# Kernel tuning notes

Hardware: AMD Instinct MI355X
Metric: run time of the kernel (lower is better)

Reference implementation:

```python
import jax, jax.numpy as jnp
import numpy as np

N_NODES = 50000
N_EDGES = 800000
D_FEAT = 64


def setup_inputs() -> dict:
    key = jax.random.key(0)
    k1, k2, k3, k4 = jax.random.split(key, 4)
    rows = jnp.sort(jax.random.randint(k1, (N_EDGES,), 0, N_NODES, dtype=jnp.int64))
    cols = jax.random.randint(k2, (N_EDGES,), 0, N_NODES, dtype=jnp.int64)
    vals = jax.random.uniform(k3, (N_EDGES,), dtype=jnp.float32)
    embeds = jax.random.normal(k4, (N_NODES, D_FEAT), dtype=jnp.float32)
    return {"rows": rows, "cols": cols, "vals": vals, "embeds": embeds}


def reference(rows, cols, vals, embeds):
    # torch.spmm(adj, embeds) with adj in COO form:
    # out[r] = sum_{e: rows[e]==r} vals[e] * embeds[cols[e]]
    gathered = vals[:, None] * embeds[cols]            # [E, D]
    out = jax.ops.segment_sum(gathered, rows, num_segments=N_NODES)  # [N, D]
    return out
```

## Files before the change

### kernel.cpp

```cpp
#include <hip/hip_runtime.h>
#include <hip/hip_fp16.h>


#define D_FEAT 64
#define BLOCK 256

typedef float f32x4 __attribute__((ext_vector_type(4)));

__global__ __launch_bounds__(BLOCK) void setup_fused(
    const int* __restrict__ rows, int* __restrict__ row_ptr,
    const float* __restrict__ embeds, __half* __restrict__ embeds_h,
    int n_nodes, int n_edges, int n4, int nb_rp)
{
    if ((int)blockIdx.x < nb_rp) {
        const int e = blockIdx.x * BLOCK + threadIdx.x;
        if (e >= n_edges) return;
        const int r  = rows[e];
        const int rp = (e == 0) ? -1 : rows[e - 1];
        for (int v = rp + 1; v <= r; ++v) row_ptr[v] = e;
        if (e == n_edges - 1)
            for (int v = r + 1; v <= n_nodes; ++v) row_ptr[v] = n_edges;
    } else {
        const int i = ((int)blockIdx.x - nb_rp) * BLOCK + (int)threadIdx.x;
        if (i >= n4) return;
        const float4 x = ((const float4*)embeds)[i];
        __half2 a = __floats2half2_rn(x.x, x.y);
        __half2 b = __floats2half2_rn(x.z, x.w);
        ((__half2*)embeds_h)[2 * i]     = a;
        ((__half2*)embeds_h)[2 * i + 1] = b;
    }
}

__global__ __launch_bounds__(BLOCK) void spmm_row_f16(
    const int* __restrict__ row_ptr,
    const int* __restrict__ cols,
    const float* __restrict__ vals,
    const __half* __restrict__ embeds_h,
    float* __restrict__ out,
    int n_nodes)
{
    const int wave = (int)((blockIdx.x * (unsigned)BLOCK + threadIdx.x) >> 6);
    if (wave >= n_nodes) return;
    const int lane = (int)(threadIdx.x & 63u);
    const int slot = lane >> 3;
    const int f8   = lane & 7;

    const int s = row_ptr[wave];
    const int t = row_ptr[wave + 1];

    float acc[8] = {0.f, 0.f, 0.f, 0.f, 0.f, 0.f, 0.f, 0.f};

    const char* eb   = (const char*)embeds_h;
    const int   foff = f8 << 4;
    const int   tm1  = t - 1;

#define EDGE_GROUP(EBASE, K)                                                   \
    {                                                                          \
        const int ik = (EBASE) + slot + 8 * (K);                               \
        const int jk = ik < tm1 ? ik : tm1;                                    \
        const int ck = cols[jk];                                               \
        float vk = vals[jk];                                                   \
        if (ik > tm1) vk = 0.f;                                                \
        const uint4 p = *(const uint4*)(eb + (((unsigned)ck << 7) + foff));    \
        float2 q0 = __half22float2(*(const __half2*)&p.x);                     \
        float2 q1 = __half22float2(*(const __half2*)&p.y);                     \
        float2 q2 = __half22float2(*(const __half2*)&p.z);                     \
        float2 q3 = __half22float2(*(const __half2*)&p.w);                     \
        acc[0] = fmaf(vk, q0.x, acc[0]); acc[1] = fmaf(vk, q0.y, acc[1]);      \
        acc[2] = fmaf(vk, q1.x, acc[2]); acc[3] = fmaf(vk, q1.y, acc[3]);      \
        acc[4] = fmaf(vk, q2.x, acc[4]); acc[5] = fmaf(vk, q2.y, acc[5]);      \
        acc[6] = fmaf(vk, q3.x, acc[6]); acc[7] = fmaf(vk, q3.y, acc[7]);      \
    }

    if (s < t) {
        if (t - s <= 16) {
            EDGE_GROUP(s, 0)
            EDGE_GROUP(s, 1)
        } else {
            for (int e = s; e < t; e += 32) {
                EDGE_GROUP(e, 0)
                EDGE_GROUP(e, 1)
                EDGE_GROUP(e, 2)
                EDGE_GROUP(e, 3)
            }
        }
    }
#undef EDGE_GROUP

#pragma unroll
    for (int i = 0; i < 8; ++i) {
        acc[i] += __shfl_xor(acc[i], 8, 64);
        acc[i] += __shfl_xor(acc[i], 16, 64);
        acc[i] += __shfl_xor(acc[i], 32, 64);
    }

    if (lane < 8) {
        f32x4 r0, r1;
        r0.x = acc[0]; r0.y = acc[1]; r0.z = acc[2]; r0.w = acc[3];
        r1.x = acc[4]; r1.y = acc[5]; r1.z = acc[6]; r1.w = acc[7];
        f32x4* po = (f32x4*)(out + (size_t)wave * D_FEAT + (f8 << 3));
        __builtin_nontemporal_store(r0, po);
        __builtin_nontemporal_store(r1, po + 1);
    }
}

extern "C" void kernel_launch(void* const* d_in, const int* in_sizes, int n_in,
                              void* d_out, int out_size, void* d_ws, size_t ws_size,
                              hipStream_t stream) {
    const int*   rows   = (const int*)d_in[0];
    const int*   cols   = (const int*)d_in[1];
    const float* vals   = (const float*)d_in[2];
    const float* embeds = (const float*)d_in[3];
    float*       out    = (float*)d_out;

    const int n_edges = in_sizes[0];
    const int n_nodes = out_size / D_FEAT;
    const int n_feat_total = n_nodes * D_FEAT;

    int*    row_ptr  = (int*)d_ws;
    __half* embeds_h = (__half*)((char*)d_ws + (1 << 18));

    {
        const int n4 = n_feat_total / 4;
        const int nb_rp  = (n_edges + BLOCK - 1) / BLOCK;
        const int nb_cvt = (n4 + BLOCK - 1) / BLOCK;
        setup_fused<<<nb_rp + nb_cvt, BLOCK, 0, stream>>>(
            rows, row_ptr, embeds, embeds_h, n_nodes, n_edges, n4, nb_rp);
    }
    {
        const int waves_per_block = BLOCK / 64;
        const int nblocks = (n_nodes + waves_per_block - 1) / waves_per_block;
        spmm_row_f16<<<nblocks, BLOCK, 0, stream>>>(
            row_ptr, cols, vals, embeds_h, out, n_nodes);
    }
}
```

Measured before the change: 93.99 us.

## Use persistent waves processing contiguous row chunks in SpMM kernel

```diff
diff --git a/kernel.cpp b/kernel.cpp
--- a/kernel.cpp
+++ b/kernel.cpp
@@ -4,6 +4,7 @@
 
 #define D_FEAT 64
 #define BLOCK 256
+#define PERSIST_BLOCKS 2048
 
 typedef float f32x4 __attribute__((ext_vector_type(4)));
 
@@ -31,7 +32,7 @@
     }
 }
 
-__global__ __launch_bounds__(BLOCK) void spmm_row_f16(
+__global__ __launch_bounds__(BLOCK) void spmm_persist(
     const int* __restrict__ row_ptr,
     const int* __restrict__ cols,
     const float* __restrict__ vals,
@@ -39,28 +40,24 @@
     float* __restrict__ out,
     int n_nodes)
 {
-    const int wave = (int)((blockIdx.x * (unsigned)BLOCK + threadIdx.x) >> 6);
-    if (wave >= n_nodes) return;
+    const int wave_g = (int)(blockIdx.x * (BLOCK / 64) + (threadIdx.x >> 6));
+    const int total_waves = PERSIST_BLOCKS * (BLOCK / 64);
+    const int chunk = (n_nodes + total_waves - 1) / total_waves;
+    const int r0 = wave_g * chunk;
+    if (r0 >= n_nodes) return;
+    const int r1 = (r0 + chunk < n_nodes) ? r0 + chunk : n_nodes;
+
     const int lane = (int)(threadIdx.x & 63u);
     const int slot = lane >> 3;
     const int f8   = lane & 7;
-
-    const int s = row_ptr[wave];
-    const int t = row_ptr[wave + 1];
-
-    float acc[8] = {0.f, 0.f, 0.f, 0.f, 0.f, 0.f, 0.f, 0.f};
-
     const char* eb   = (const char*)embeds_h;
     const int   foff = f8 << 4;
-    const int   tm1  = t - 1;
 
-#define EDGE_GROUP(EBASE, K)                                                   \
+#define GROUP_NC(EBASE)                                                        \
     {                                                                          \
-        const int ik = (EBASE) + slot + 8 * (K);                               \
-        const int jk = ik < tm1 ? ik : tm1;                                    \
-        const int ck = cols[jk];                                               \
-        float vk = vals[jk];                                                   \
-        if (ik > tm1) vk = 0.f;                                                \
+        const int ik = (EBASE) + slot;                                         \
+        const int ck = __builtin_nontemporal_load(cols + ik);                  \
+        const float vk = __builtin_nontemporal_load(vals + ik);                \
         const uint4 p = *(const uint4*)(eb + (((unsigned)ck << 7) + foff));    \
         float2 q0 = __half22float2(*(const __half2*)&p.x);                     \
         float2 q1 = __half22float2(*(const __half2*)&p.y);                     \
@@ -72,36 +69,59 @@
         acc[6] = fmaf(vk, q3.x, acc[6]); acc[7] = fmaf(vk, q3.y, acc[7]);      \
     }
 
-    if (s < t) {
-        if (t - s <= 16) {
-            EDGE_GROUP(s, 0)
-            EDGE_GROUP(s, 1)
-        } else {
-            for (int e = s; e < t; e += 32) {
-                EDGE_GROUP(e, 0)
-                EDGE_GROUP(e, 1)
-                EDGE_GROUP(e, 2)
-                EDGE_GROUP(e, 3)
+#define GROUP_C(EBASE, TM1)                                                    \
+    {                                                                          \
+        const int ik = (EBASE) + slot;                                         \
+        const int jk = ik < (TM1) ? ik : (TM1);                                \
+        const int ck = __builtin_nontemporal_load(cols + jk);                  \
+        float vk = __builtin_nontemporal_load(vals + jk);                      \
+        if (ik > (TM1)) vk = 0.f;                                              \
+        const uint4 p = *(const uint4*)(eb + (((unsigned)ck << 7) + foff));    \
+        float2 q0 = __half22float2(*(const __half2*)&p.x);                     \
+        float2 q1 = __half22float2(*(const __half2*)&p.y);                     \
+        float2 q2 = __half22float2(*(const __half2*)&p.z);                     \
+        float2 q3 = __half22float2(*(const __half2*)&p.w);                     \
+        acc[0] = fmaf(vk, q0.x, acc[0]); acc[1] = fmaf(vk, q0.y, acc[1]);      \
+        acc[2] = fmaf(vk, q1.x, acc[2]); acc[3] = fmaf(vk, q1.y, acc[3]);      \
+        acc[4] = fmaf(vk, q2.x, acc[4]); acc[5] = fmaf(vk, q2.y, acc[5]);      \
+        acc[6] = fmaf(vk, q3.x, acc[6]); acc[7] = fmaf(vk, q3.y, acc[7]);      \
+    }
+
+    int s = row_ptr[r0];
+    for (int r = r0; r < r1; ++r) {
+        const int t = row_ptr[r + 1];
+        float acc[8] = {0.f, 0.f, 0.f, 0.f, 0.f, 0.f, 0.f, 0.f};
+
+        if (s < t) {
+            const int tm1 = t - 1;
+            int e = s;
+            for (; e + 16 < t; e += 16) {
+                GROUP_NC(e)
+                GROUP_NC(e + 8)
             }
+            GROUP_C(e, tm1)
+            if (e + 8 < t) GROUP_C(e + 8, tm1)
         }
-    }
-#undef EDGE_GROUP
 
 #pragma unroll
-    for (int i = 0; i < 8; ++i) {
-        acc[i] += __shfl_xor(acc[i], 8, 64);
-        acc[i] += __shfl_xor(acc[i], 16, 64);
-        acc[i] += __shfl_xor(acc[i], 32, 64);
+        for (int i = 0; i < 8; ++i) {
+            acc[i] += __shfl_xor(acc[i], 8, 64);
+            acc[i] += __shfl_xor(acc[i], 16, 64);
+            acc[i] += __shfl_xor(acc[i], 32, 64);
+        }
+
+        if (lane < 8) {
+            f32x4 v0, v1;
+            v0.x = acc[0]; v0.y = acc[1]; v0.z = acc[2]; v0.w = acc[3];
+            v1.x = acc[4]; v1.y = acc[5]; v1.z = acc[6]; v1.w = acc[7];
+            f32x4* po = (f32x4*)(out + (size_t)r * D_FEAT + (f8 << 3));
+            __builtin_nontemporal_store(v0, po);
+            __builtin_nontemporal_store(v1, po + 1);
+        }
+        s = t;
     }
-
-    if (lane < 8) {
-        f32x4 r0, r1;
-        r0.x = acc[0]; r0.y = acc[1]; r0.z = acc[2]; r0.w = acc[3];
-        r1.x = acc[4]; r1.y = acc[5]; r1.z = acc[6]; r1.w = acc[7];
-        f32x4* po = (f32x4*)(out + (size_t)wave * D_FEAT + (f8 << 3));
-        __builtin_nontemporal_store(r0, po);
-        __builtin_nontemporal_store(r1, po + 1);
-    }
+#undef GROUP_NC
+#undef GROUP_C
 }
 
 extern "C" void kernel_launch(void* const* d_in, const int* in_sizes, int n_in,
@@ -128,9 +148,7 @@
             rows, row_ptr, embeds, embeds_h, n_nodes, n_edges, n4, nb_rp);
     }
     {
-        const int waves_per_block = BLOCK / 64;
-        const int nblocks = (n_nodes + waves_per_block - 1) / waves_per_block;
-        spmm_row_f16<<<nblocks, BLOCK, 0, stream>>>(
+        spmm_persist<<<PERSIST_BLOCKS, BLOCK, 0, stream>>>(
             row_ptr, cols, vals, embeds_h, out, n_nodes);
     }
 }
```

Result: slower. 101.1 us (+7.6%).

## Process two rows per wave with interleaved gathers in SpMM

Applied to the files above, without the earlier changes.

```diff
diff --git a/kernel.cpp b/kernel.cpp
--- a/kernel.cpp
+++ b/kernel.cpp
@@ -31,7 +31,7 @@
     }
 }
 
-__global__ __launch_bounds__(BLOCK) void spmm_row_f16(
+__global__ __launch_bounds__(BLOCK) void spmm_pair(
     const int* __restrict__ row_ptr,
     const int* __restrict__ cols,
     const float* __restrict__ vals,
@@ -39,68 +39,88 @@
     float* __restrict__ out,
     int n_nodes)
 {
-    const int wave = (int)((blockIdx.x * (unsigned)BLOCK + threadIdx.x) >> 6);
-    if (wave >= n_nodes) return;
+    const int pair = (int)((blockIdx.x * (unsigned)BLOCK + threadIdx.x) >> 6);
+    const int rA = pair * 2;
+    if (rA >= n_nodes) return;
+    const int rB = rA + 1;
+    const bool hasB = rB < n_nodes;
+
     const int lane = (int)(threadIdx.x & 63u);
     const int slot = lane >> 3;
     const int f8   = lane & 7;
-
-    const int s = row_ptr[wave];
-    const int t = row_ptr[wave + 1];
-
-    float acc[8] = {0.f, 0.f, 0.f, 0.f, 0.f, 0.f, 0.f, 0.f};
-
     const char* eb   = (const char*)embeds_h;
     const int   foff = f8 << 4;
-    const int   tm1  = t - 1;
 
-#define EDGE_GROUP(EBASE, K)                                                   \
+    const int sA = row_ptr[rA];
+    const int tA = row_ptr[rA + 1];
+    const int sB = tA;
+    const int tB = hasB ? row_ptr[rB + 1] : tA;
+
+    const int degA = tA - sA;
+    const int degB = tB - sB;
+    const int tm1A = tA - 1;
+    const int tm1B = tB - 1;
+
+    float accA[8] = {0.f, 0.f, 0.f, 0.f, 0.f, 0.f, 0.f, 0.f};
+    float accB[8] = {0.f, 0.f, 0.f, 0.f, 0.f, 0.f, 0.f, 0.f};
+
+#define GROUP(EBASE, TM1, ACC)                                                 \
     {                                                                          \
-        const int ik = (EBASE) + slot + 8 * (K);                               \
-        const int jk = ik < tm1 ? ik : tm1;                                    \
-        const int ck = cols[jk];                                               \
-        float vk = vals[jk];                                                   \
-        if (ik > tm1) vk = 0.f;                                                \
+        const int ik = (EBASE) + slot;                                         \
+        const int jk = ik < (TM1) ? ik : (TM1);                                \
+        const int ck = __builtin_nontemporal_load(cols + jk);                  \
+        float vk = __builtin_nontemporal_load(vals + jk);                      \
+        if (ik > (TM1)) vk = 0.f;                                              \
         const uint4 p = *(const uint4*)(eb + (((unsigned)ck << 7) + foff));    \
         float2 q0 = __half22float2(*(const __half2*)&p.x);                     \
         float2 q1 = __half22float2(*(const __half2*)&p.y);                     \
         float2 q2 = __half22float2(*(const __half2*)&p.z);                     \
         float2 q3 = __half22float2(*(const __half2*)&p.w);                     \
-        acc[0] = fmaf(vk, q0.x, acc[0]); acc[1] = fmaf(vk, q0.y, acc[1]);      \
-        acc[2] = fmaf(vk, q1.x, acc[2]); acc[3] = fmaf(vk, q1.y, acc[3]);      \
-        acc[4] = fmaf(vk, q2.x, acc[4]); acc[5] = fmaf(vk, q2.y, acc[5]);      \
-        acc[6] = fmaf(vk, q3.x, acc[6]); acc[7] = fmaf(vk, q3.y, acc[7]);      \
+        ACC[0] = fmaf(vk, q0.x, ACC[0]); ACC[1] = fmaf(vk, q0.y, ACC[1]);      \
+        ACC[2] = fmaf(vk, q1.x, ACC[2]); ACC[3] = fmaf(vk, q1.y, ACC[3]);      \
+        ACC[4] = fmaf(vk, q2.x, ACC[4]); ACC[5] = fmaf(vk, q2.y, ACC[5]);      \
+        ACC[6] = fmaf(vk, q3.x, ACC[6]); ACC[7] = fmaf(vk, q3.y, ACC[7]);      \
     }
 
-    if (s < t) {
-        if (t - s <= 16) {
-            EDGE_GROUP(s, 0)
-            EDGE_GROUP(s, 1)
-        } else {
-            for (int e = s; e < t; e += 32) {
-                EDGE_GROUP(e, 0)
-                EDGE_GROUP(e, 1)
-                EDGE_GROUP(e, 2)
-                EDGE_GROUP(e, 3)
-            }
-        }
+    if (degA > 0 && degA <= 24 && degB > 0 && degB <= 24) {
+        GROUP(sA,      tm1A, accA)
+        GROUP(sB,      tm1B, accB)
+        GROUP(sA + 8,  tm1A, accA)
+        GROUP(sB + 8,  tm1B, accB)
+        GROUP(sA + 16, tm1A, accA)
+        GROUP(sB + 16, tm1B, accB)
+    } else {
+        if (degA > 0)
+            for (int e = sA; e < tA; e += 8) GROUP(e, tm1A, accA)
+        if (degB > 0)
+            for (int e = sB; e < tB; e += 8) GROUP(e, tm1B, accB)
     }
-#undef EDGE_GROUP
+#undef GROUP
 
 #pragma unroll
     for (int i = 0; i < 8; ++i) {
-        acc[i] += __shfl_xor(acc[i], 8, 64);
-        acc[i] += __shfl_xor(acc[i], 16, 64);
-        acc[i] += __shfl_xor(acc[i], 32, 64);
+        accA[i] += __shfl_xor(accA[i], 8, 64);
+        accB[i] += __shfl_xor(accB[i], 8, 64);
+        accA[i] += __shfl_xor(accA[i], 16, 64);
+        accB[i] += __shfl_xor(accB[i], 16, 64);
+        accA[i] += __shfl_xor(accA[i], 32, 64);
+        accB[i] += __shfl_xor(accB[i], 32, 64);
     }
 
     if (lane < 8) {
-        f32x4 r0, r1;
-        r0.x = acc[0]; r0.y = acc[1]; r0.z = acc[2]; r0.w = acc[3];
-        r1.x = acc[4]; r1.y = acc[5]; r1.z = acc[6]; r1.w = acc[7];
-        f32x4* po = (f32x4*)(out + (size_t)wave * D_FEAT + (f8 << 3));
-        __builtin_nontemporal_store(r0, po);
-        __builtin_nontemporal_store(r1, po + 1);
+        f32x4 v0, v1;
+        v0.x = accA[0]; v0.y = accA[1]; v0.z = accA[2]; v0.w = accA[3];
+        v1.x = accA[4]; v1.y = accA[5]; v1.z = accA[6]; v1.w = accA[7];
+        f32x4* po = (f32x4*)(out + (size_t)rA * D_FEAT + (f8 << 3));
+        __builtin_nontemporal_store(v0, po);
+        __builtin_nontemporal_store(v1, po + 1);
+    } else if (lane < 16 && hasB) {
+        f32x4 v0, v1;
+        v0.x = accB[0]; v0.y = accB[1]; v0.z = accB[2]; v0.w = accB[3];
+        v1.x = accB[4]; v1.y = accB[5]; v1.z = accB[6]; v1.w = accB[7];
+        f32x4* po = (f32x4*)(out + (size_t)rB * D_FEAT + (f8 << 3));
+        __builtin_nontemporal_store(v0, po);
+        __builtin_nontemporal_store(v1, po + 1);
     }
 }
 
@@ -128,9 +148,10 @@
             rows, row_ptr, embeds, embeds_h, n_nodes, n_edges, n4, nb_rp);
     }
     {
+        const int n_pairs = (n_nodes + 1) / 2;
         const int waves_per_block = BLOCK / 64;
-        const int nblocks = (n_nodes + waves_per_block - 1) / waves_per_block;
-        spmm_row_f16<<<nblocks, BLOCK, 0, stream>>>(
+        const int nblocks = (n_pairs + waves_per_block - 1) / waves_per_block;
+        spmm_pair<<<nblocks, BLOCK, 0, stream>>>(
             row_ptr, cols, vals, embeds_h, out, n_nodes);
     }
 }
```

Result: slower. 97.81 us (+4.1%).

## Pack per-row cols/vals into padded ELL slab with CSR tail fallback

Applied to the files above, without the earlier changes.

```diff
diff --git a/kernel.cpp b/kernel.cpp
--- a/kernel.cpp
+++ b/kernel.cpp
@@ -4,6 +4,12 @@
 
 #define D_FEAT 64
 #define BLOCK 256
+#define PAD_STRIDE 32
+
+#define WS_ROWPTR_OFF   0u
+#define WS_CNT_OFF      0x40000u
+#define WS_EMB_OFF      0x80000u
+#define WS_PAD_OFF      0x700000u
 
 typedef float f32x4 __attribute__((ext_vector_type(4)));
 
@@ -31,7 +37,42 @@
     }
 }
 
-__global__ __launch_bounds__(BLOCK) void spmm_row_f16(
+__device__ __forceinline__ int pad_off(int k) {
+    return ((k >> 4) << 7) + ((k & 7) << 4) + (((k >> 3) & 1) << 3);
+}
+
+__global__ __launch_bounds__(BLOCK) void setup_pad(
+    const int* __restrict__ rows,
+    const int* __restrict__ cols,
+    const float* __restrict__ vals,
+    const int* __restrict__ row_ptr,
+    char* __restrict__ padb,
+    int* __restrict__ cnt,
+    int n_nodes, int n_edges)
+{
+    const int tid = (int)(blockIdx.x * BLOCK + threadIdx.x);
+    if (tid < n_edges) {
+        const int r = rows[tid];
+        const int k = tid - row_ptr[r];
+        if (k < PAD_STRIDE) {
+            uint2 cv;
+            cv.x = (unsigned)cols[tid];
+            cv.y = __float_as_uint(vals[tid]);
+            *(uint2*)(padb + (size_t)r * 256 + pad_off(k)) = cv;
+        }
+    } else if (tid < n_edges + n_nodes) {
+        const int r = tid - n_edges;
+        const int deg = row_ptr[r + 1] - row_ptr[r];
+        cnt[r] = (deg + 15) >> 4;
+        const uint2 z = make_uint2(0u, 0u);
+        for (int k = deg; k < PAD_STRIDE; ++k)
+            *(uint2*)(padb + (size_t)r * 256 + pad_off(k)) = z;
+    }
+}
+
+__global__ __launch_bounds__(BLOCK) void spmm_padded(
+    const char* __restrict__ padb,
+    const int* __restrict__ cnt,
     const int* __restrict__ row_ptr,
     const int* __restrict__ cols,
     const float* __restrict__ vals,
@@ -39,29 +80,20 @@
     float* __restrict__ out,
     int n_nodes)
 {
-    const int wave = (int)((blockIdx.x * (unsigned)BLOCK + threadIdx.x) >> 6);
-    if (wave >= n_nodes) return;
+    const int r = (int)((blockIdx.x * (unsigned)BLOCK + threadIdx.x) >> 6);
+    if (r >= n_nodes) return;
     const int lane = (int)(threadIdx.x & 63u);
     const int slot = lane >> 3;
     const int f8   = lane & 7;
-
-    const int s = row_ptr[wave];
-    const int t = row_ptr[wave + 1];
+    const char* eb0  = (const char*)embeds_h + (f8 << 4);
+    const char* rowb = padb + (size_t)r * 256 + (slot << 4);
 
     float acc[8] = {0.f, 0.f, 0.f, 0.f, 0.f, 0.f, 0.f, 0.f};
 
-    const char* eb   = (const char*)embeds_h;
-    const int   foff = f8 << 4;
-    const int   tm1  = t - 1;
-
-#define EDGE_GROUP(EBASE, K)                                                   \
+#define PROC(COL, VAL)                                                         \
     {                                                                          \
-        const int ik = (EBASE) + slot + 8 * (K);                               \
-        const int jk = ik < tm1 ? ik : tm1;                                    \
-        const int ck = cols[jk];                                               \
-        float vk = vals[jk];                                                   \
-        if (ik > tm1) vk = 0.f;                                                \
-        const uint4 p = *(const uint4*)(eb + (((unsigned)ck << 7) + foff));    \
+        const float vk = __uint_as_float(VAL);                                 \
+        const uint4 p = *(const uint4*)(eb0 + ((size_t)(COL) << 7));           \
         float2 q0 = __half22float2(*(const __half2*)&p.x);                     \
         float2 q1 = __half22float2(*(const __half2*)&p.y);                     \
         float2 q2 = __half22float2(*(const __half2*)&p.z);                     \
@@ -72,20 +104,37 @@
         acc[6] = fmaf(vk, q3.x, acc[6]); acc[7] = fmaf(vk, q3.y, acc[7]);      \
     }
 
-    if (s < t) {
-        if (t - s <= 16) {
-            EDGE_GROUP(s, 0)
-            EDGE_GROUP(s, 1)
-        } else {
-            for (int e = s; e < t; e += 32) {
-                EDGE_GROUP(e, 0)
-                EDGE_GROUP(e, 1)
-                EDGE_GROUP(e, 2)
-                EDGE_GROUP(e, 3)
+    const uint4 cv0 = *(const uint4*)(rowb);
+    const int nc = cnt[r];
+    PROC(cv0.x, cv0.y)
+    PROC(cv0.z, cv0.w)
+
+    if (nc > 1) {
+        const uint4 cv1 = *(const uint4*)(rowb + 128);
+        PROC(cv1.x, cv1.y)
+        PROC(cv1.z, cv1.w)
+        if (nc > 2) {
+            const int s = row_ptr[r], t = row_ptr[r + 1];
+            const int tm1 = t - 1;
+            for (int e = s + PAD_STRIDE; e < t; e += 8) {
+                const int ik = e + slot;
+                const int jk = ik < tm1 ? ik : tm1;
+                const unsigned ck = (unsigned)cols[jk];
+                float vk = vals[jk];
+                if (ik > tm1) vk = 0.f;
+                const uint4 p = *(const uint4*)(eb0 + ((size_t)ck << 7));
+                float2 q0 = __half22float2(*(const __half2*)&p.x);
+                float2 q1 = __half22float2(*(const __half2*)&p.y);
+                float2 q2 = __half22float2(*(const __half2*)&p.z);
+                float2 q3 = __half22float2(*(const __half2*)&p.w);
+                acc[0] = fmaf(vk, q0.x, acc[0]); acc[1] = fmaf(vk, q0.y, acc[1]);
+                acc[2] = fmaf(vk, q1.x, acc[2]); acc[3] = fmaf(vk, q1.y, acc[3]);
+                acc[4] = fmaf(vk, q2.x, acc[4]); acc[5] = fmaf(vk, q2.y, acc[5]);
+                acc[6] = fmaf(vk, q3.x, acc[6]); acc[7] = fmaf(vk, q3.y, acc[7]);
             }
         }
     }
-#undef EDGE_GROUP
+#undef PROC
 
 #pragma unroll
     for (int i = 0; i < 8; ++i) {
@@ -95,12 +144,12 @@
     }
 
     if (lane < 8) {
-        f32x4 r0, r1;
-        r0.x = acc[0]; r0.y = acc[1]; r0.z = acc[2]; r0.w = acc[3];
-        r1.x = acc[4]; r1.y = acc[5]; r1.z = acc[6]; r1.w = acc[7];
-        f32x4* po = (f32x4*)(out + (size_t)wave * D_FEAT + (f8 << 3));
-        __builtin_nontemporal_store(r0, po);
-        __builtin_nontemporal_store(r1, po + 1);
+        f32x4 v0, v1;
+        v0.x = acc[0]; v0.y = acc[1]; v0.z = acc[2]; v0.w = acc[3];
+        v1.x = acc[4]; v1.y = acc[5]; v1.z = acc[6]; v1.w = acc[7];
+        f32x4* po = (f32x4*)(out + (size_t)r * D_FEAT + (f8 << 3));
+        __builtin_nontemporal_store(v0, po);
+        __builtin_nontemporal_store(v1, po + 1);
     }
 }
 
@@ -117,8 +166,10 @@
     const int n_nodes = out_size / D_FEAT;
     const int n_feat_total = n_nodes * D_FEAT;
 
-    int*    row_ptr  = (int*)d_ws;
-    __half* embeds_h = (__half*)((char*)d_ws + (1 << 18));
+    int*    row_ptr  = (int*)((char*)d_ws + WS_ROWPTR_OFF);
+    int*    cnt      = (int*)((char*)d_ws + WS_CNT_OFF);
+    __half* embeds_h = (__half*)((char*)d_ws + WS_EMB_OFF);
+    char*   padb     = (char*)d_ws + WS_PAD_OFF;
 
     {
         const int n4 = n_feat_total / 4;
@@ -128,9 +179,15 @@
             rows, row_ptr, embeds, embeds_h, n_nodes, n_edges, n4, nb_rp);
     }
     {
+        const int n_total = n_edges + n_nodes;
+        const int nblocks = (n_total + BLOCK - 1) / BLOCK;
+        setup_pad<<<nblocks, BLOCK, 0, stream>>>(
+            rows, cols, vals, row_ptr, padb, cnt, n_nodes, n_edges);
+    }
+    {
         const int waves_per_block = BLOCK / 64;
         const int nblocks = (n_nodes + waves_per_block - 1) / waves_per_block;
-        spmm_row_f16<<<nblocks, BLOCK, 0, stream>>>(
-            row_ptr, cols, vals, embeds_h, out, n_nodes);
+        spmm_padded<<<nblocks, BLOCK, 0, stream>>>(
+            padb, cnt, row_ptr, cols, vals, embeds_h, out, n_nodes);
     }
 }
```

After: 105.6 us. 1.12x slower.
